# Kernel tuning notes

Hardware: AMD Instinct MI355X
Metric: run time of the kernel (lower is better)

The kernel has to match this reference:

```python
import jax, jax.numpy as jnp
import numpy as np

B, CIN, COUT, H, W = 4, 256, 256, 64, 64
K, G = 3, 4
PAD = (K - 1) // 2


def setup_inputs() -> dict:
    key = jax.random.key(0)
    k0, k1, k2, k3 = jax.random.split(key, 4)
    x = jax.random.normal(k0, (B, CIN, H, W), jnp.float32)
    y = jax.random.normal(k1, (B, 2, H, W), jnp.float32)
    # conv_offset: 1x1 conv, no bias, init std=0.1 (normal_init)
    w_offset = jax.random.normal(k2, (G * 2 * K * K, 2, 1, 1), jnp.float32) * 0.1
    # DeformConv2d weight, no bias, init std=0.01
    w_deform = jax.random.normal(k3, (COUT, CIN, K, K), jnp.float32) * 0.01
    return {"x": x, "y": y, "w_offset": w_offset, "w_deform": w_deform}


def _deform_conv(x, offset, weight):
    """DCN v1: stride 1, dilation 1, zero padding PAD, deform_groups=G, groups=1."""
    KK = K * K
    # mmcv offset layout: [B, G*2*KK, H, W] -> per group, per kernel pos, (dy, dx)
    off = offset.reshape(B, G, KK, 2, H, W)
    dy, dx = off[:, :, :, 0], off[:, :, :, 1]            # [B,G,KK,H,W]
    ii, jj = jnp.meshgrid(jnp.arange(K), jnp.arange(K), indexing="ij")
    ky = ii.reshape(KK).astype(x.dtype)                  # kernel row offsets
    kx = jj.reshape(KK).astype(x.dtype)                  # kernel col offsets
    base_y = jnp.arange(H, dtype=x.dtype)[None, :, None] - PAD + ky[:, None, None]  # [KK,H,1]
    base_x = jnp.arange(W, dtype=x.dtype)[None, None, :] - PAD + kx[:, None, None]  # [KK,1,W]
    yc = dy + base_y                                     # [B,G,KK,H,W]
    xc = dx + base_x

    Cg = CIN // G
    xg = x.reshape(B, G, Cg, H, W)

    def sample(xg1, yc1, xc1):
        # xg1 [Cg,H,W]; yc1/xc1 [KK,H,W] -> bilinear sample with zero padding
        y0 = jnp.floor(yc1)
        x0 = jnp.floor(xc1)
        wy = yc1 - y0
        wx = xc1 - x0
        y0i = y0.astype(jnp.int32)
        x0i = x0.astype(jnp.int32)

        def gather(yi, xi):
            valid = (yi >= 0) & (yi < H) & (xi >= 0) & (xi < W)
            v = xg1[:, jnp.clip(yi, 0, H - 1), jnp.clip(xi, 0, W - 1)]  # [Cg,KK,H,W]
            return v * valid[None].astype(xg1.dtype)

        v00 = gather(y0i, x0i)
        v01 = gather(y0i, x0i + 1)
        v10 = gather(y0i + 1, x0i)
        v11 = gather(y0i + 1, x0i + 1)
        return (v00 * (1 - wy) * (1 - wx) + v01 * (1 - wy) * wx
                + v10 * wy * (1 - wx) + v11 * wy * wx)

    sampled = jax.vmap(jax.vmap(sample))(xg, yc, xc)     # [B,G,Cg,KK,H,W]
    sampled = sampled.reshape(B, CIN, KK, H, W)
    wflat = weight.reshape(COUT, CIN, KK)
    return jnp.einsum("bckhw,ock->bohw", sampled, wflat)  # [B,COUT,H,W]


def reference(x, y, w_offset, w_deform):
    # offset = conv_offset(y.detach()), a 1x1 conv without bias
    y_det = jax.lax.stop_gradient(y)
    offset = jnp.einsum("bihw,oi->bohw", y_det, w_offset[:, :, 0, 0])
    out = _deform_conv(x, offset, w_deform)
    return jax.nn.relu(out)
```

## Files before the change

### kernel.cpp

```cpp
#include <hip/hip_runtime.h>
#include <cstddef>

#define B_    4
#define CIN_  256
#define COUT_ 256
#define H_    64
#define W_    64
#define KK_   9
#define G_    4
#define PAD_  1
#define NSL   36

typedef short bf16x8 __attribute__((ext_vector_type(8)));
typedef float f32x4  __attribute__((ext_vector_type(4)));
typedef __attribute__((address_space(1))) const unsigned int* gptr_t;
typedef __attribute__((address_space(3))) unsigned int*       lptr_t;

__device__ __forceinline__ unsigned short f2bf(float v) {
    unsigned int u = __float_as_uint(v);
    u += 0x7fffu + ((u >> 16) & 1u);
    return (unsigned short)(u >> 16);
}
__device__ __forceinline__ float f_lo(unsigned int u) { return __uint_as_float(u << 16); }
__device__ __forceinline__ float f_hi(unsigned int u) { return __uint_as_float(u & 0xffff0000u); }

__global__ __launch_bounds__(256) void prep_kernel(const float* __restrict__ x,
                                                   unsigned short* __restrict__ xT,
                                                   const float* __restrict__ w,
                                                   unsigned short* __restrict__ wb) {
    const int tid = threadIdx.x;
    if (blockIdx.x < 512) {
        __shared__ unsigned short s[128][66];
        const int bh    = blockIdx.x >> 1;
        const int chalf = blockIdx.x & 1;
        const size_t src_base = ((size_t)(bh >> 6) * CIN_ + chalf * 128) * (H_ * W_) + (bh & 63) * W_;
        #pragma unroll 4
        for (int k = 0; k < 32; ++k) {
            int i = k * 256 + tid;
            int c = i >> 6, ww = i & 63;
            s[c][ww] = f2bf(x[src_base + (size_t)c * (H_ * W_) + ww]);
        }
        __syncthreads();
        #pragma unroll 4
        for (int k = 0; k < 16; ++k) {
            int j  = k * 256 + tid;
            int c2 = (j & 63) * 2, ww = j >> 6;
            unsigned int lo = s[c2][ww], hi = s[c2 + 1][ww];
            *(unsigned int*)(xT + ((size_t)bh * 64 + ww) * 256 + chalf * 128 + c2) = lo | (hi << 16);
        }
    } else {
        int idx = (blockIdx.x - 512) * 256 + tid;
        int e   = idx & 7;
        int pos = (idx >> 3) & 7;
        int o   = (idx >> 6) & 255;
        int t   = idx >> 14;
        int g   = t / 9, kk = t - g * 9;
        int j   = pos ^ (o & 7);
        int c   = g * 64 + j * 8 + e;
        wb[idx] = f2bf(w[(o * CIN_ + c) * KK_ + kk]);
    }
}

__global__ __launch_bounds__(512, 2) void dcn_kernel(
    const unsigned short* __restrict__ xT, const float* __restrict__ y,
    const float* __restrict__ w_off, const unsigned short* __restrict__ wb,
    float* __restrict__ out)
{
    __shared__ unsigned short s_W[2][COUT_ * 64];
    __shared__ unsigned short s_S[2][64 * 64];

    const int tid = threadIdx.x;
    const int bid = blockIdx.x;
    const int xcd = bid & 7;
    const int b   = xcd >> 1;
    const int h   = (xcd & 1) * 32 + (bid >> 3);

    const int sp = tid >> 3;
    const int c8 = tid & 7;

    const float yv0 = y[((b * 2 + 0) * H_ + h) * W_ + sp];
    const float yv1 = y[((b * 2 + 1) * H_ + h) * W_ + sp];

    const int lane = tid & 63, wave = tid >> 6;
    const int pg  = wave & 1, oh = wave >> 1;
    const int l15 = lane & 15, kq = lane >> 4, sw = l15 & 7;

    f32x4 acc[8];
    #pragma unroll
    for (int i = 0; i < 8; ++i) acc[i] = (f32x4){0.f, 0.f, 0.f, 0.f};

    const size_t xbase = (size_t)b * (H_ * W_ * 256) + c8 * 8;

    float w00, w01, w10, w11;
    uint4 A, Bv, C, D;

#define ISSUE_SAMPLE(t) do {                                                   \
    const int g_ = (t) / 9, kk_ = (t) % 9;                                     \
    const float4 co = *(const float4*)(w_off + (t) * 4);                       \
    const float dy = fmaf(yv0, co.x, yv1 * co.y);                              \
    const float dx = fmaf(yv0, co.z, yv1 * co.w);                              \
    const float yc = (float)(h + (kk_ / 3) - PAD_) + dy;                       \
    const float xc = (float)(sp + (kk_ % 3) - PAD_) + dx;                      \
    const float yf = floorf(yc), xf = floorf(xc);                              \
    const float wy = yc - yf,    wx = xc - xf;                                 \
    const int   yi = (int)yf,    xi = (int)xf;                                 \
    float a00 = (1.f - wy) * (1.f - wx);                                       \
    float a01 = (1.f - wy) * wx;                                               \
    float a10 = wy * (1.f - wx);                                               \
    float a11 = wy * wx;                                                       \
    const bool y0ok = (yi >= 0) & (yi < H_);                                   \
    const bool y1ok = (yi >= -1) & (yi < H_ - 1);                              \
    const bool x0ok = (xi >= 0) & (xi < W_);                                   \
    const bool x1ok = (xi >= -1) & (xi < W_ - 1);                              \
    w00 = (y0ok & x0ok) ? a00 : 0.f;                                           \
    w01 = (y0ok & x1ok) ? a01 : 0.f;                                           \
    w10 = (y1ok & x0ok) ? a10 : 0.f;                                           \
    w11 = (y1ok & x1ok) ? a11 : 0.f;                                           \
    const int y0c = min(max(yi, 0), H_ - 1);                                   \
    const int y1c = min(max(yi + 1, 0), H_ - 1);                               \
    const int x0c = min(max(xi, 0), W_ - 1);                                   \
    const int x1c = min(max(xi + 1, 0), W_ - 1);                               \
    const unsigned short* xb = xT + xbase + g_ * 64;                           \
    A  = *(const uint4*)(xb + ((size_t)y0c * W_ + x0c) * 256);                 \
    Bv = *(const uint4*)(xb + ((size_t)y0c * W_ + x1c) * 256);                 \
    C  = *(const uint4*)(xb + ((size_t)y1c * W_ + x0c) * 256);                 \
    D  = *(const uint4*)(xb + ((size_t)y1c * W_ + x1c) * 256);                 \
} while (0)

#define STAGE_W(t, buf) do {                                                   \
    const unsigned short* src = wb + (size_t)(t) * 16384;                      \
    _Pragma("unroll")                                                          \
    for (int j = 0; j < 4; ++j) {                                              \
        const int off = (j * 512 + tid) * 8;                                   \
        __builtin_amdgcn_global_load_lds((gptr_t)(src + off),                  \
                                         (lptr_t)(s_W[buf] + off), 16, 0, 0);  \
    }                                                                          \
} while (0)

#define WRITE_SAMPLE(buf) do {                                                 \
    const unsigned int av[4] = {A.x, A.y, A.z, A.w};                           \
    const unsigned int bv[4] = {Bv.x, Bv.y, Bv.z, Bv.w};                       \
    const unsigned int cv[4] = {C.x, C.y, C.z, C.w};                           \
    const unsigned int dv[4] = {D.x, D.y, D.z, D.w};                           \
    unsigned int res[4];                                                       \
    _Pragma("unroll")                                                          \
    for (int q = 0; q < 4; ++q) {                                              \
        float rl = w00 * f_lo(av[q]);                                          \
        rl = fmaf(w01, f_lo(bv[q]), rl);                                       \
        rl = fmaf(w10, f_lo(cv[q]), rl);                                       \
        rl = fmaf(w11, f_lo(dv[q]), rl);                                       \
        float rh = w00 * f_hi(av[q]);                                          \
        rh = fmaf(w01, f_hi(bv[q]), rh);                                       \
        rh = fmaf(w10, f_hi(cv[q]), rh);                                       \
        rh = fmaf(w11, f_hi(dv[q]), rh);                                       \
        res[q] = __builtin_amdgcn_perm(__float_as_uint(rh),                    \
                                       __float_as_uint(rl), 0x07060302u);      \
    }                                                                          \
    *(uint4*)(s_S[buf] + sp * 64 + ((c8 ^ (sp & 7)) * 8)) =                    \
        make_uint4(res[0], res[1], res[2], res[3]);                            \
} while (0)

#define MFMA_STEP(buf) do {                                                    \
    bf16x8 bf[2][2], af[2][4];                                                 \
    _Pragma("unroll")                                                          \
    for (int kh = 0; kh < 2; ++kh) {                                           \
        const int pos = ((kh * 4 + kq) ^ sw) * 8;                              \
        _Pragma("unroll")                                                      \
        for (int nt = 0; nt < 2; ++nt)                                         \
            bf[kh][nt] = *(const bf16x8*)(s_S[buf] +                           \
                              (pg * 32 + nt * 16 + l15) * 64 + pos);           \
        _Pragma("unroll")                                                      \
        for (int mt = 0; mt < 4; ++mt)                                         \
            af[kh][mt] = *(const bf16x8*)(s_W[buf] +                           \
                              (oh * 64 + mt * 16 + l15) * 64 + pos);           \
    }                                                                          \
    __builtin_amdgcn_s_setprio(1);                                             \
    _Pragma("unroll")                                                          \
    for (int kh = 0; kh < 2; ++kh)                                             \
        _Pragma("unroll")                                                      \
        for (int nt = 0; nt < 2; ++nt)                                         \
            _Pragma("unroll")                                                  \
            for (int mt = 0; mt < 4; ++mt)                                     \
                acc[nt * 4 + mt] = __builtin_amdgcn_mfma_f32_16x16x32_bf16(    \
                    af[kh][mt], bf[kh][nt], acc[nt * 4 + mt], 0, 0, 0);        \
    __builtin_amdgcn_s_setprio(0);                                             \
} while (0)

    ISSUE_SAMPLE(0);
    STAGE_W(0, 0);
    WRITE_SAMPLE(0);
    __syncthreads();

    for (int s = 0; s < NSL; s += 2) {
        ISSUE_SAMPLE(s + 1);
        STAGE_W(s + 1, 1);
        __builtin_amdgcn_sched_barrier(0);
        MFMA_STEP(0);
        WRITE_SAMPLE(1);
        __syncthreads();

        if (s + 2 < NSL) {
            ISSUE_SAMPLE(s + 2);
            STAGE_W(s + 2, 0);
        }
        __builtin_amdgcn_sched_barrier(0);
        MFMA_STEP(1);
        if (s + 2 < NSL) WRITE_SAMPLE(0);
        __syncthreads();
    }

    #pragma unroll
    for (int nt = 0; nt < 2; ++nt) {
        const int px = pg * 32 + nt * 16 + l15;
        #pragma unroll
        for (int mt = 0; mt < 4; ++mt) {
            const int obase = oh * 64 + mt * 16 + kq * 4;
            #pragma unroll
            for (int r = 0; r < 4; ++r) {
                out[(((size_t)b * COUT_ + obase + r) * H_ + h) * W_ + px] =
                    fmaxf(acc[nt * 4 + mt][r], 0.f);
            }
        }
    }
#undef ISSUE_SAMPLE
#undef STAGE_W
#undef WRITE_SAMPLE
#undef MFMA_STEP
}

extern "C" void kernel_launch(void* const* d_in, const int* in_sizes, int n_in,
                              void* d_out, int out_size, void* d_ws, size_t ws_size,
                              hipStream_t stream) {
    const float* x     = (const float*)d_in[0];
    const float* y     = (const float*)d_in[1];
    const float* w_off = (const float*)d_in[2];
    const float* w_def = (const float*)d_in[3];
    float* out = (float*)d_out;

    unsigned short* xT = (unsigned short*)d_ws;
    unsigned short* wb = (unsigned short*)d_ws + 4194304;

    prep_kernel<<<2816, 256, 0, stream>>>(x, xT, w_def, wb);
    dcn_kernel<<<256, 512, 0, stream>>>(xT, y, w_off, wb, out);
}
```

Baseline: 122.0 us.

## Triple-buffer weight tiles and prefetch two slices ahead with explicit barriers

```diff
diff --git a/kernel.cpp b/kernel.cpp
--- a/kernel.cpp
+++ b/kernel.cpp
@@ -66,7 +66,7 @@
     const float* __restrict__ w_off, const unsigned short* __restrict__ wb,
     float* __restrict__ out)
 {
-    __shared__ unsigned short s_W[2][COUT_ * 64];
+    __shared__ unsigned short s_W[3][COUT_ * 64];
     __shared__ unsigned short s_S[2][64 * 64];
 
     const int tid = threadIdx.x;
@@ -133,7 +133,7 @@
     for (int j = 0; j < 4; ++j) {                                              \
         const int off = (j * 512 + tid) * 8;                                   \
         __builtin_amdgcn_global_load_lds((gptr_t)(src + off),                  \
-                                         (lptr_t)(s_W[buf] + off), 16, 0, 0);  \
+                                         (lptr_t)(s_W[buf] + off), 16, 0, 0); \
     }                                                                          \
 } while (0)
 
@@ -160,18 +160,18 @@
         make_uint4(res[0], res[1], res[2], res[3]);                            \
 } while (0)
 
-#define MFMA_STEP(buf) do {                                                    \
+#define MFMA_STEP(wb_, sb_) do {                                               \
     bf16x8 bf[2][2], af[2][4];                                                 \
     _Pragma("unroll")                                                          \
     for (int kh = 0; kh < 2; ++kh) {                                           \
         const int pos = ((kh * 4 + kq) ^ sw) * 8;                              \
         _Pragma("unroll")                                                      \
         for (int nt = 0; nt < 2; ++nt)                                         \
-            bf[kh][nt] = *(const bf16x8*)(s_S[buf] +                           \
+            bf[kh][nt] = *(const bf16x8*)(s_S[sb_] +                           \
                               (pg * 32 + nt * 16 + l15) * 64 + pos);           \
         _Pragma("unroll")                                                      \
         for (int mt = 0; mt < 4; ++mt)                                         \
-            af[kh][mt] = *(const bf16x8*)(s_W[buf] +                           \
+            af[kh][mt] = *(const bf16x8*)(s_W[wb_] +                           \
                               (oh * 64 + mt * 16 + l15) * 64 + pos);           \
     }                                                                          \
     __builtin_amdgcn_s_setprio(1);                                             \
@@ -186,28 +186,50 @@
     __builtin_amdgcn_s_setprio(0);                                             \
 } while (0)
 
+#define STEP(s_, WCUR, WPRE, SCUR, SNXT, DO_ISS, DO_STG, DO_BAR) do {          \
+    if (DO_ISS) ISSUE_SAMPLE((s_) + 1);                                        \
+    __builtin_amdgcn_sched_barrier(0);                                         \
+    if (DO_STG) STAGE_W((s_) + 2, WPRE);                                       \
+    __builtin_amdgcn_sched_barrier(0);                                         \
+    MFMA_STEP(WCUR, SCUR);                                                     \
+    __builtin_amdgcn_sched_barrier(0);                                         \
+    if (DO_ISS) WRITE_SAMPLE(SNXT);                                            \
+    __builtin_amdgcn_sched_barrier(0);                                         \
+    if (DO_BAR) {                                                              \
+        asm volatile("s_waitcnt lgkmcnt(0)" ::: "memory");                     \
+        __builtin_amdgcn_sched_barrier(0);                                     \
+        __builtin_amdgcn_s_barrier();                                          \
+        __builtin_amdgcn_sched_barrier(0);                                     \
+    }                                                                          \
+} while (0)
+
     ISSUE_SAMPLE(0);
+    __builtin_amdgcn_sched_barrier(0);
     STAGE_W(0, 0);
+    __builtin_amdgcn_sched_barrier(0);
     WRITE_SAMPLE(0);
-    __syncthreads();
-
-    for (int s = 0; s < NSL; s += 2) {
-        ISSUE_SAMPLE(s + 1);
-        STAGE_W(s + 1, 1);
-        __builtin_amdgcn_sched_barrier(0);
-        MFMA_STEP(0);
-        WRITE_SAMPLE(1);
-        __syncthreads();
-
-        if (s + 2 < NSL) {
-            ISSUE_SAMPLE(s + 2);
-            STAGE_W(s + 2, 0);
-        }
-        __builtin_amdgcn_sched_barrier(0);
-        MFMA_STEP(1);
-        if (s + 2 < NSL) WRITE_SAMPLE(0);
-        __syncthreads();
+    __builtin_amdgcn_sched_barrier(0);
+    STAGE_W(1, 1);
+    __builtin_amdgcn_sched_barrier(0);
+    asm volatile("s_waitcnt vmcnt(4) lgkmcnt(0)" ::: "memory");
+    __builtin_amdgcn_sched_barrier(0);
+    __builtin_amdgcn_s_barrier();
+    __builtin_amdgcn_sched_barrier(0);
+
+    for (int sb = 0; sb < 30; sb += 6) {
+        STEP(sb + 0, 0, 2, 0, 1, 1, 1, 1);
+        STEP(sb + 1, 1, 0, 1, 0, 1, 1, 1);
+        STEP(sb + 2, 2, 1, 0, 1, 1, 1, 1);
+        STEP(sb + 3, 0, 2, 1, 0, 1, 1, 1);
+        STEP(sb + 4, 1, 0, 0, 1, 1, 1, 1);
+        STEP(sb + 5, 2, 1, 1, 0, 1, 1, 1);
     }
+    STEP(30, 0, 2, 0, 1, 1, 1, 1);
+    STEP(31, 1, 0, 1, 0, 1, 1, 1);
+    STEP(32, 2, 1, 0, 1, 1, 1, 1);
+    STEP(33, 0, 2, 1, 0, 1, 1, 1);
+    STEP(34, 1, 0, 0, 1, 1, 0, 1);
+    STEP(35, 2, 1, 1, 0, 0, 0, 0);
 
     #pragma unroll
     for (int nt = 0; nt < 2; ++nt) {
@@ -226,6 +248,7 @@
 #undef STAGE_W
 #undef WRITE_SAMPLE
 #undef MFMA_STEP
+#undef STEP
 }
 
 extern "C" void kernel_launch(void* const* d_in, const int* in_sizes, int n_in,
```

Result: no change. 121.5 us (-0.4%).
